# Kernel tuning notes

Measured on AMD Instinct MI355X. Metric: run time of the kernel, lower is better.

Reference implementation:

```python
import jax, jax.numpy as jnp
import numpy as np

N = 100000      # nodes
E = 1600000     # edges (avg degree 16)
F_IN = 128      # num_features
H = 128         # hidden_channels
OUT = 64        # out_channels


def _glorot(key, shape):
    lim = float(np.sqrt(6.0 / (shape[0] + shape[1])))
    return jax.random.uniform(key, shape, jnp.float32, -lim, lim)


def setup_inputs() -> dict:
    key = jax.random.key(0)
    ks = jax.random.split(key, 5)
    x = jax.random.normal(ks[0], (N, F_IN), jnp.float32)
    edge_index = jax.random.randint(ks[1], (2, E), 0, N, dtype=jnp.int64)
    W1 = _glorot(ks[2], (F_IN, H)); b1 = jnp.zeros((H,), jnp.float32)
    W2 = _glorot(ks[3], (H, H));    b2 = jnp.zeros((H,), jnp.float32)
    W3 = _glorot(ks[4], (H, OUT));  b3 = jnp.zeros((OUT,), jnp.float32)
    return {"x": x, "edge_index": edge_index,
            "W1": W1, "b1": b1, "W2": W2, "b2": b2, "W3": W3, "b3": b3}


def _gcn_conv(h, src, dst, norm, W, b, n):
    # PyG GCNConv: linear transform, then sym-normalized scatter aggregation, then bias
    h = h @ W                                   # [N, d_out]
    msg = h[src] * norm[:, None]                # gather + scale, [E+N, d_out]
    agg = jax.ops.segment_sum(msg, dst, num_segments=n)
    return agg + b


def reference(x, edge_index, W1, b1, W2, b2, W3, b3):
    n = x.shape[0]
    # add self-loops (GCNConv default add_self_loops=True)
    loop = jnp.arange(n, dtype=edge_index.dtype)
    src = jnp.concatenate([edge_index[0], loop])
    dst = jnp.concatenate([edge_index[1], loop])
    # symmetric normalization deg^-1/2[src] * deg^-1/2[dst]
    deg = jax.ops.segment_sum(jnp.ones_like(dst, x.dtype), dst, num_segments=n)
    dinv = jnp.where(deg > 0, jax.lax.rsqrt(deg), 0.0)
    norm = dinv[src] * dinv[dst]

    h = jax.nn.relu(_gcn_conv(x, src, dst, norm, W1, b1, n))  # dropout p=0 -> no-op
    h = jax.nn.relu(_gcn_conv(h, src, dst, norm, W2, b2, n))
    h = _gcn_conv(h, src, dst, norm, W3, b3, n)
    return jax.nn.log_softmax(h, axis=1)
```

## Files before the change

### kernel.cpp

```cpp
#include <hip/hip_runtime.h>
#include <stdint.h>
#include <math.h>

#define FIN 128

typedef __attribute__((ext_vector_type(8))) short short8v;
typedef __attribute__((ext_vector_type(4))) float float4v;
typedef __attribute__((ext_vector_type(2))) float float2v;

__device__ __forceinline__ uint32_t f2_to_bf2(float x, float y) {
    uint32_t r;
    asm("v_cvt_pk_bf16_f32 %0, %1, %2" : "=v"(r) : "v"(x), "v"(y));
    return r;
}
__device__ __forceinline__ unsigned short f_to_bf(float x) {
    union { float f; uint32_t i; } a;
    a.f = x;
    uint32_t u = a.i + 0x7FFF + ((a.i >> 16) & 1);
    return (unsigned short)(u >> 16);
}
__device__ __forceinline__ void acc16_fp8_pk(float2v* acc2, uint4 v) {
    uint32_t us[4] = {v.x, v.y, v.z, v.w};
#pragma unroll
    for (int q = 0; q < 4; ++q) {
        acc2[q * 2 + 0] += __builtin_amdgcn_cvt_pk_f32_fp8(us[q], false);
        acc2[q * 2 + 1] += __builtin_amdgcn_cvt_pk_f32_fp8(us[q], true);
    }
}

__device__ __forceinline__ int edge_at(const void* ei, long long idx, int is32) {
    return is32 ? ((const int*)ei)[idx] : (int)((const long long*)ei)[idx];
}

#define SP_CHUNK 4096
__global__ __launch_bounds__(256) void splitA_kernel(const void* __restrict__ ei,
                                                     int* __restrict__ gCnt,
                                                     uint32_t* __restrict__ buf1,
                                                     int E, int capS) {
    __shared__ int hist[16];
    __shared__ int gbase[16];
    __shared__ int lflag;
    int t = threadIdx.x;
    if (t < 16) hist[t] = 0;
    if (t == 0) lflag = 0;
    long long base = (long long)blockIdx.x * SP_CHUNK;
    __syncthreads();
    {
        long long e = base + t;
        if (e < E && ((const int*)ei)[2 * e + 1] != 0) atomicOr(&lflag, 1);
    }
    __syncthreads();
    int is32 = lflag;
    uint32_t lrec[16], rec[16];
#pragma unroll
    for (int j = 0; j < 16; ++j) {
        long long e = base + t + j * 256;
        if (e < E) {
            int s = edge_at(ei, e, is32);
            int d = edge_at(ei, (long long)E + e, is32);
            int b = d >> 13;
            int lofs = atomicAdd(&hist[b], 1);
            lrec[j] = ((uint32_t)lofs << 4) | (uint32_t)b;
            rec[j] = ((uint32_t)s << 13) | (uint32_t)(d & 8191);
        } else
            lrec[j] = 0xFFFFFFFFu;
    }
    __syncthreads();
    if (t < 16) gbase[t] = atomicAdd(&gCnt[t], hist[t]);
    __syncthreads();
#pragma unroll
    for (int j = 0; j < 16; ++j) {
        if (lrec[j] != 0xFFFFFFFFu) {
            int b = lrec[j] & 15;
            int pos = gbase[b] + (int)(lrec[j] >> 4);
            if (pos < capS) buf1[(size_t)b * capS + pos] = rec[j];
        }
    }
}

__global__ __launch_bounds__(256) void splitB_kernel(const int* __restrict__ gCnt,
                                                     const uint32_t* __restrict__ buf1,
                                                     int* __restrict__ cnt2,
                                                     uint32_t* __restrict__ buf2,
                                                     int capS, int cap2, int NB) {
    __shared__ int hist[128];
    __shared__ int gbase[128];
    int t = threadIdx.x;
    int s = blockIdx.y;
    if (t < 128) hist[t] = 0;
    __syncthreads();
    int m = gCnt[s];
    if (m > capS) m = capS;
    long long base = (long long)blockIdx.x * SP_CHUNK;
    uint32_t lrec[16], r32[16];
#pragma unroll
    for (int j = 0; j < 16; ++j) {
        long long i = base + t + j * 256;
        if (i < m) {
            uint32_t r = buf1[(size_t)s * capS + i];
            int d13 = (int)(r & 8191u);
            int sub = d13 >> 6;
            int lofs = atomicAdd(&hist[sub], 1);
            lrec[j] = ((uint32_t)lofs << 7) | (uint32_t)sub;
            r32[j] = ((r >> 13) << 6) | (uint32_t)(d13 & 63);
        } else
            lrec[j] = 0xFFFFFFFFu;
    }
    __syncthreads();
    if (t < 128) {
        int g = s * 128 + t;
        gbase[t] = (g < NB) ? atomicAdd(&cnt2[g], hist[t]) : 0;
    }
    __syncthreads();
#pragma unroll
    for (int j = 0; j < 16; ++j) {
        if (lrec[j] != 0xFFFFFFFFu) {
            int sub = lrec[j] & 127;
            int pos = gbase[sub] + (int)(lrec[j] >> 7);
            if (pos < cap2) buf2[(size_t)(s * 128 + sub) * cap2 + pos] = r32[j];
        }
    }
}

__global__ __launch_bounds__(256) void binBC_kernel(const int* __restrict__ cnt2,
                                                    const uint32_t* __restrict__ buf2,
                                                    int* __restrict__ cnt,
                                                    float* __restrict__ dinv,
                                                    int* __restrict__ rowend,
                                                    int* __restrict__ col,
                                                    int n, int cap2) {
    __shared__ int h[64];
    __shared__ int rowst[64];
    __shared__ int cur[64];
    __shared__ int sc[64];
    int bin = blockIdx.x;
    int t = threadIdx.x;
    if (t < 64) { h[t] = 0; cur[t] = 0; }
    __syncthreads();
    int m = cnt2[bin];
    if (m > cap2) m = cap2;
    const uint32_t* buf = buf2 + (size_t)bin * cap2;
    for (int i = t; i < m; i += 256) atomicAdd(&h[buf[i] & 63], 1);
    __syncthreads();
    int c = 0;
    if (t < 64) { c = h[t]; sc[t] = c; }
    __syncthreads();
    for (int off = 1; off < 64; off <<= 1) {
        int v = 0;
        if (t < 64 && t >= off) v = sc[t - off];
        __syncthreads();
        if (t < 64) sc[t] += v;
        __syncthreads();
    }
    if (t < 64) {
        int node = bin * 64 + t;
        int base = bin * cap2;
        rowst[t] = base + sc[t] - c;
        if (node < n) {
            cnt[node] = c;
            dinv[node] = rsqrtf((float)c + 1.0f);
            rowend[node] = base + sc[t];
        }
    }
    __syncthreads();
    for (int i = t; i < m; i += 256) {
        uint32_t rec = buf[i];
        int d6 = rec & 63;
        int off = atomicAdd(&cur[d6], 1);
        col[rowst[d6] + off] = (int)(rec >> 6);
    }
}

__global__ __launch_bounds__(256) void wconv_all(const float* __restrict__ W1,
                                                 const float* __restrict__ W2,
                                                 const float* __restrict__ W3,
                                                 unsigned short* __restrict__ Wf1,
                                                 unsigned short* __restrict__ Wf2,
                                                 unsigned short* __restrict__ Wf3) {
    int idx = blockIdx.x * 256 + threadIdx.x;
    const float* W;
    unsigned short* Wf;
    int NCOL, base;
    if (idx < 2048)      { W = W1; Wf = Wf1; NCOL = 128; base = idx; }
    else if (idx < 4096) { W = W2; Wf = Wf2; NCOL = 128; base = idx - 2048; }
    else if (idx < 5120) { W = W3; Wf = Wf3; NCOL = 64;  base = idx - 4096; }
    else return;
    int f = base >> 6, l = base & 63;
    int ct = f >> 2, ks = f & 3;
    int nn = ct * 16 + (l & 15);
    int k0 = ks * 32 + (l >> 4) * 8;
    uint32_t pk[4];
#pragma unroll
    for (int j = 0; j < 4; ++j) {
        float a = W[(size_t)(k0 + 2 * j) * NCOL + nn];
        float b = W[(size_t)(k0 + 2 * j + 1) * NCOL + nn];
        pk[j] = f2_to_bf2(a, b);
    }
    uint4 v = make_uint4(pk[0], pk[1], pk[2], pk[3]);
    ((uint4*)Wf)[base] = v;
}

template <int NCOL, int A_FP32, int OUT_FP8>
__global__ __launch_bounds__(256) void gemm_mfma(const void* __restrict__ Av,
                                                 const unsigned short* __restrict__ Wf,
                                                 const float* __restrict__ dinv,
                                                 void* __restrict__ Cv, int n) {
    __shared__ unsigned short lds[NCOL * 128];
    const int t = threadIdx.x;
    for (int i = t; i < NCOL * 16; i += 256)
        ((uint4*)lds)[i] = ((const uint4*)Wf)[i];
    __syncthreads();

    const int wave = t >> 6, lane = t & 63;
    const int row0 = blockIdx.x * 64 + wave * 16;
    const int m = lane & 15, quad = lane >> 4;
    int arow = row0 + m;
    if (arow >= n) arow = n - 1;

    short8v a[4];
    if (A_FP32) {
        const float* A = (const float*)Av;
#pragma unroll
        for (int ks = 0; ks < 4; ++ks) {
            float4 lo = *(const float4*)(A + (size_t)arow * 128 + ks * 32 + quad * 8);
            float4 hi = *(const float4*)(A + (size_t)arow * 128 + ks * 32 + quad * 8 + 4);
            union { short8v v; uint32_t u[4]; } pk;
            pk.u[0] = f2_to_bf2(lo.x, lo.y);
            pk.u[1] = f2_to_bf2(lo.z, lo.w);
            pk.u[2] = f2_to_bf2(hi.x, hi.y);
            pk.u[3] = f2_to_bf2(hi.z, hi.w);
            a[ks] = pk.v;
        }
    } else {
        const unsigned short* A = (const unsigned short*)Av;
#pragma unroll
        for (int ks = 0; ks < 4; ++ks)
            a[ks] = *(const short8v*)(A + (size_t)arow * 128 + ks * 32 + quad * 8);
    }

    const int cr0 = row0 + quad * 4;
    float ds[4];
#pragma unroll
    for (int r = 0; r < 4; ++r) {
        int gr = cr0 + r;
        ds[r] = (gr < n) ? dinv[gr] : 0.0f;
    }
#pragma unroll
    for (int ct = 0; ct < NCOL / 16; ++ct) {
        float4v acc = {0.0f, 0.0f, 0.0f, 0.0f};
#pragma unroll
        for (int ks = 0; ks < 4; ++ks) {
            int f = ct * 4 + ks;
            short8v b = *(const short8v*)(lds + ((size_t)(f * 64 + lane)) * 8);
            acc = __builtin_amdgcn_mfma_f32_16x16x32_bf16(a[ks], b, acc, 0, 0, 0);
        }
#pragma unroll
        for (int r = 0; r < 4; ++r) {
            int gr = cr0 + r;
            if (gr < n) {
                float val = acc[r] * ds[r];
                if (OUT_FP8) {
                    int u = __builtin_amdgcn_cvt_pk_fp8_f32(val, val, 0, false);
                    ((unsigned char*)Cv)[(size_t)gr * NCOL + ct * 16 + m] =
                        (unsigned char)(u & 0xFF);
                } else {
                    ((unsigned short*)Cv)[(size_t)gr * NCOL + ct * 16 + m] = f_to_bf(val);
                }
            }
        }
    }
}

__global__ __launch_bounds__(256) void agg_relu_128_fp8(
        const uint32_t* __restrict__ T8, const int* __restrict__ rowend,
        const int* __restrict__ cnt, const int* __restrict__ col,
        const float* __restrict__ dinv, const float* __restrict__ bias,
        uint32_t* __restrict__ outHb, int n) {
    int wid = blockIdx.x * 4 + (threadIdx.x >> 6);
    int lane = threadIdx.x & 63;
    int sel = lane >> 5, slot = (lane >> 3) & 3, j = lane & 7;
    int nodeA = wid * 2;
    int node = nodeA + sel;
    if (nodeA >= n) return;
    bool valid = node < n;
    int nd = valid ? node : nodeA;
    int end = rowend[nd];
    int start = end - cnt[nd];
    if (!valid) start = end;

    float2v acc2[8];
#pragma unroll
    for (int k = 0; k < 8; ++k) acc2[k] = (float2v){0.0f, 0.0f};
    if (slot == 0 && valid) {
        uint4 v = *(const uint4*)(T8 + (size_t)node * 32 + j * 4);
        acc16_fp8_pk(acc2, v);
    }
    int deg = end - start;
    int degM = max(deg, __shfl_xor(deg, 32, 64));
    int p = start + slot;
    const int ZR = n;
    for (int it = 0; it < degM; it += 8) {
        int e0 = p, e1 = p + 4;
        int s0 = col[e0], s1 = col[e1];
        if (e0 >= end) s0 = ZR;
        if (e1 >= end) s1 = ZR;
        uint4 v0 = *(const uint4*)(T8 + (size_t)s0 * 32 + j * 4);
        uint4 v1 = *(const uint4*)(T8 + (size_t)s1 * 32 + j * 4);
        acc16_fp8_pk(acc2, v0);
        acc16_fp8_pk(acc2, v1);
        p += 8;
    }
    float* acc = (float*)acc2;
#pragma unroll
    for (int k = 0; k < 16; ++k) {
        acc[k] += __shfl_xor(acc[k], 8, 64);
        acc[k] += __shfl_xor(acc[k], 16, 64);
    }
    if (slot == 0 && valid) {
        float di = dinv[node];
        const float4* b4 = (const float4*)bias;
        float r[16];
#pragma unroll
        for (int q = 0; q < 4; ++q) {
            float4 bb = b4[j * 4 + q];
            r[q * 4 + 0] = fmaxf(di * acc[q * 4 + 0] + bb.x, 0.0f);
            r[q * 4 + 1] = fmaxf(di * acc[q * 4 + 1] + bb.y, 0.0f);
            r[q * 4 + 2] = fmaxf(di * acc[q * 4 + 2] + bb.z, 0.0f);
            r[q * 4 + 3] = fmaxf(di * acc[q * 4 + 3] + bb.w, 0.0f);
        }
        uint4 o0, o1;
        o0.x = f2_to_bf2(r[0], r[1]);   o0.y = f2_to_bf2(r[2], r[3]);
        o0.z = f2_to_bf2(r[4], r[5]);   o0.w = f2_to_bf2(r[6], r[7]);
        o1.x = f2_to_bf2(r[8], r[9]);   o1.y = f2_to_bf2(r[10], r[11]);
        o1.z = f2_to_bf2(r[12], r[13]); o1.w = f2_to_bf2(r[14], r[15]);
        *(uint4*)(outHb + (size_t)node * 64 + j * 8) = o0;
        *(uint4*)(outHb + (size_t)node * 64 + j * 8 + 4) = o1;
    }
}

__global__ __launch_bounds__(256) void agg_lsm_64_fp8(
        const uint32_t* __restrict__ T8, const int* __restrict__ rowend,
        const int* __restrict__ cnt, const int* __restrict__ col,
        const float* __restrict__ dinv, const float* __restrict__ bias,
        float* __restrict__ out, int n) {
    int wid = blockIdx.x * 4 + (threadIdx.x >> 6);
    int lane = threadIdx.x & 63;
    int sel = lane >> 5, slot = (lane >> 2) & 7, j = lane & 3;
    int nodeA = wid * 2;
    int node = nodeA + sel;
    if (nodeA >= n) return;
    bool valid = node < n;
    int nd = valid ? node : nodeA;
    int end = rowend[nd];
    int start = end - cnt[nd];
    if (!valid) start = end;

    float2v acc2[8];
#pragma unroll
    for (int k = 0; k < 8; ++k) acc2[k] = (float2v){0.0f, 0.0f};
    if (slot == 0 && valid) {
        uint4 v = *(const uint4*)(T8 + (size_t)node * 16 + j * 4);
        acc16_fp8_pk(acc2, v);
    }
    int deg = end - start;
    int degM = max(deg, __shfl_xor(deg, 32, 64));
    int p = start + slot;
    const int ZR = 2 * n;
    for (int it = 0; it < degM; it += 16) {
        int e0 = p, e1 = p + 8;
        int s0 = col[e0], s1 = col[e1];
        if (e0 >= end) s0 = ZR;
        if (e1 >= end) s1 = ZR;
        uint4 v0 = *(const uint4*)(T8 + (size_t)s0 * 16 + j * 4);
        uint4 v1 = *(const uint4*)(T8 + (size_t)s1 * 16 + j * 4);
        acc16_fp8_pk(acc2, v0);
        acc16_fp8_pk(acc2, v1);
        p += 16;
    }
    float* acc = (float*)acc2;
#pragma unroll
    for (int k = 0; k < 16; ++k) {
        acc[k] += __shfl_xor(acc[k], 4, 64);
        acc[k] += __shfl_xor(acc[k], 8, 64);
        acc[k] += __shfl_xor(acc[k], 16, 64);
    }
    float di = dinv[nd];
    const float4* b4 = (const float4*)bias;
    float r[16];
#pragma unroll
    for (int q = 0; q < 4; ++q) {
        float4 bb = b4[j * 4 + q];
        r[q * 4 + 0] = di * acc[q * 4 + 0] + bb.x;
        r[q * 4 + 1] = di * acc[q * 4 + 1] + bb.y;
        r[q * 4 + 2] = di * acc[q * 4 + 2] + bb.z;
        r[q * 4 + 3] = di * acc[q * 4 + 3] + bb.w;
    }
    float m8[8];
#pragma unroll
    for (int q = 0; q < 8; ++q) m8[q] = fmaxf(r[2 * q], r[2 * q + 1]);
#pragma unroll
    for (int q = 0; q < 4; ++q) m8[q] = fmaxf(m8[q], m8[q + 4]);
    float m = fmaxf(fmaxf(m8[0], m8[2]), fmaxf(m8[1], m8[3]));
    m = fmaxf(m, __shfl_xor(m, 1, 64));
    m = fmaxf(m, __shfl_xor(m, 2, 64));
    float e[16];
#pragma unroll
    for (int k = 0; k < 16; ++k) e[k] = __expf(r[k] - m);
#pragma unroll
    for (int q = 0; q < 8; ++q) e[q] += e[q + 8];
#pragma unroll
    for (int q = 0; q < 4; ++q) e[q] += e[q + 4];
    float ss = (e[0] + e[2]) + (e[1] + e[3]);
    ss += __shfl_xor(ss, 1, 64);
    ss += __shfl_xor(ss, 2, 64);
    float lg = m + __logf(ss);
    if (slot == 0 && valid) {
#pragma unroll
        for (int q = 0; q < 4; ++q) {
            float4 o = make_float4(r[q * 4 + 0] - lg, r[q * 4 + 1] - lg,
                                   r[q * 4 + 2] - lg, r[q * 4 + 3] - lg);
            *(float4*)(out + (size_t)node * 64 + j * 16 + q * 4) = o;
        }
    }
}

extern "C" void kernel_launch(void* const* d_in, const int* in_sizes, int n_in,
                              void* d_out, int out_size, void* d_ws, size_t ws_size,
                              hipStream_t stream) {
    const float* x  = (const float*)d_in[0];
    const void*  ei = d_in[1];
    const float* W1 = (const float*)d_in[2];
    const float* b1 = (const float*)d_in[3];
    const float* W2 = (const float*)d_in[4];
    const float* b2 = (const float*)d_in[5];
    const float* W3 = (const float*)d_in[6];
    const float* b3 = (const float*)d_in[7];
    float* out = (float*)d_out;

    const int n = in_sizes[0] / FIN;
    const int E = in_sizes[1] / 2;

    char* p = (char*)d_ws;
    auto carve = [&](size_t bytes) {
        char* q = p;
        p += (bytes + 255) & ~(size_t)255;
        return q;
    };
    const int NB = (n + 63) / 64;
    const int NS = (n + 8191) / 8192;

    long long meanS = (long long)E * 8192 / n;
    int capS = (int)(meanS + 8 * (long long)sqrt((double)meanS) + 1024);
    capS = (capS + 15) & ~15;
    long long mean2 = (long long)E * 64 / n;
    int cap2 = (int)(mean2 + 8 * (long long)sqrt((double)mean2) + 64);
    cap2 = (cap2 + 15) & ~15;

    int*   cnt     = (int*)carve((size_t)n * 4);
    int*   rowend  = (int*)carve((size_t)n * 4);
    float* dinv    = (float*)carve((size_t)n * 4);
    int*   colb    = (int*)carve(((size_t)NB * cap2 + 4096) * 4);
    int*   gCnt    = (int*)carve((size_t)(16 + NB) * 4);
    int*   cnt2    = gCnt + 16;
    size_t Tbytes = (size_t)n * 128 + 256;
    size_t Hbytes = (size_t)n * 128 * 2;
    char*  TH = carve(Tbytes + Hbytes);
    void*  T  = (void*)TH;
    unsigned short* Hb = (unsigned short*)(TH + Tbytes);
    unsigned short* Wf1 = (unsigned short*)carve(128 * 128 * 2);
    unsigned short* Wf2 = (unsigned short*)carve(128 * 128 * 2);
    unsigned short* Wf3 = (unsigned short*)carve(128 * 64 * 2);

    size_t buf1B = ((size_t)NS * capS * 4 + 255) & ~(size_t)255;
    uint32_t* buf1 = (uint32_t*)TH;
    uint32_t* buf2 = (uint32_t*)(TH + buf1B);
    size_t avail2 = (Tbytes + Hbytes > buf1B) ? (Tbytes + Hbytes - buf1B) : 0;
    size_t maxc2 = avail2 / ((size_t)NB * 4);
    if ((size_t)cap2 > maxc2) cap2 = (int)maxc2;

    hipMemsetAsync(gCnt, 0, (size_t)(16 + NB) * 4, stream);

    const int gagg2 = ((n + 1) / 2 + 3) / 4;
    const int ggemm = (n + 63) / 64;
    const int gsplitA = (E + SP_CHUNK - 1) / SP_CHUNK;
    const int gsplitBx = (capS + SP_CHUNK - 1) / SP_CHUNK;

    splitA_kernel<<<gsplitA, 256, 0, stream>>>(ei, gCnt, buf1, E, capS);
    splitB_kernel<<<dim3(gsplitBx, NS), 256, 0, stream>>>(gCnt, buf1, cnt2, buf2, capS,
                                                          cap2, NB);
    binBC_kernel<<<NB, 256, 0, stream>>>(cnt2, buf2, cnt, dinv, rowend, colb, n, cap2);
    hipMemsetAsync(TH + (size_t)n * 128, 0, 128, stream);
    wconv_all<<<20, 256, 0, stream>>>(W1, W2, W3, Wf1, Wf2, Wf3);

    gemm_mfma<128, 1, 1><<<ggemm, 256, 0, stream>>>(x, Wf1, dinv, T, n);
    agg_relu_128_fp8<<<gagg2, 256, 0, stream>>>((const uint32_t*)T, rowend, cnt, colb,
                                                dinv, b1, (uint32_t*)Hb, n);
    gemm_mfma<128, 0, 1><<<ggemm, 256, 0, stream>>>(Hb, Wf2, dinv, T, n);
    agg_relu_128_fp8<<<gagg2, 256, 0, stream>>>((const uint32_t*)T, rowend, cnt, colb,
                                                dinv, b2, (uint32_t*)Hb, n);
    gemm_mfma<64, 0, 1><<<ggemm, 256, 0, stream>>>(Hb, Wf3, dinv, T, n);
    agg_lsm_64_fp8<<<gagg2, 256, 0, stream>>>((const uint32_t*)T, rowend, cnt, colb,
                                              dinv, b3, out, n);
}
```

Before: 297.8 us.

## Store self-loop and pad CSR rows to multiples of four, regather aggregation lanes

The CSR build now puts each node's self-loop into its own column list and pads every row to a multiple of four with a zero-row index, so cnt includes the self-loop and dinv uses rsqrt(cnt). The aggregation kernels loop over padded rows with no per-edge bounds checks and no separate self-term load. Lanes are remapped to two or four edge slots with 8-byte gathers, and the slot reduction uses DPP and ds_swizzle instead of shuffles. The zero row is now written by the GEMM kernel instead of a memset, and cap2 grows to hold the padding, which costs extra column storage and some padded gather work.

Measured after the change: 323.1 us. +8.5%, slower.

```diff
diff --git a/kernel.cpp b/kernel.cpp
--- a/kernel.cpp
+++ b/kernel.cpp
@@ -19,13 +19,22 @@
     uint32_t u = a.i + 0x7FFF + ((a.i >> 16) & 1);
     return (unsigned short)(u >> 16);
 }
-__device__ __forceinline__ void acc16_fp8_pk(float2v* acc2, uint4 v) {
-    uint32_t us[4] = {v.x, v.y, v.z, v.w};
-#pragma unroll
-    for (int q = 0; q < 4; ++q) {
-        acc2[q * 2 + 0] += __builtin_amdgcn_cvt_pk_f32_fp8(us[q], false);
-        acc2[q * 2 + 1] += __builtin_amdgcn_cvt_pk_f32_fp8(us[q], true);
-    }
+__device__ __forceinline__ void acc8_fp8_pk(float2v* acc2, uint2 v) {
+    acc2[0] += __builtin_amdgcn_cvt_pk_f32_fp8(v.x, false);
+    acc2[1] += __builtin_amdgcn_cvt_pk_f32_fp8(v.x, true);
+    acc2[2] += __builtin_amdgcn_cvt_pk_f32_fp8(v.y, false);
+    acc2[3] += __builtin_amdgcn_cvt_pk_f32_fp8(v.y, true);
+}
+
+template <int CTRL>
+__device__ __forceinline__ float dppmov(float x) {
+    int i = __builtin_bit_cast(int, x);
+    int r = __builtin_amdgcn_update_dpp(i, i, CTRL, 0xF, 0xF, false);
+    return __builtin_bit_cast(float, r);
+}
+__device__ __forceinline__ float swz16f(float x) {
+    int r = __builtin_amdgcn_ds_swizzle(__builtin_bit_cast(int, x), 0x401F);
+    return __builtin_bit_cast(float, r);
 }
 
 __device__ __forceinline__ int edge_at(const void* ei, long long idx, int is32) {
@@ -126,7 +135,7 @@
                                                     const uint32_t* __restrict__ buf2,
                                                     int* __restrict__ cnt,
                                                     float* __restrict__ dinv,
-                                                    int* __restrict__ rowend,
+                                                    int* __restrict__ rowstart,
                                                     int* __restrict__ col,
                                                     int n, int cap2) {
     __shared__ int h[64];
@@ -135,15 +144,18 @@
     __shared__ int sc[64];
     int bin = blockIdx.x;
     int t = threadIdx.x;
-    if (t < 64) { h[t] = 0; cur[t] = 0; }
+    if (t < 64) {
+        h[t] = (bin * 64 + t < n) ? 1 : 0;
+        cur[t] = 1;
+    }
     __syncthreads();
     int m = cnt2[bin];
     if (m > cap2) m = cap2;
     const uint32_t* buf = buf2 + (size_t)bin * cap2;
     for (int i = t; i < m; i += 256) atomicAdd(&h[buf[i] & 63], 1);
     __syncthreads();
-    int c = 0;
-    if (t < 64) { c = h[t]; sc[t] = c; }
+    int c = 0, pc = 0;
+    if (t < 64) { c = h[t]; pc = (c + 3) & ~3; sc[t] = pc; }
     __syncthreads();
     for (int off = 1; off < 64; off <<= 1) {
         int v = 0;
@@ -155,11 +167,14 @@
     if (t < 64) {
         int node = bin * 64 + t;
         int base = bin * cap2;
-        rowst[t] = base + sc[t] - c;
+        int st = base + sc[t] - pc;
+        rowst[t] = st;
         if (node < n) {
             cnt[node] = c;
-            dinv[node] = rsqrtf((float)c + 1.0f);
-            rowend[node] = base + sc[t];
+            dinv[node] = rsqrtf((float)c);
+            rowstart[node] = st;
+            col[st] = node;
+            for (int k = c; k < pc; ++k) col[st + k] = n;
         }
     }
     __syncthreads();
@@ -207,6 +222,8 @@
                                                  void* __restrict__ Cv, int n) {
     __shared__ unsigned short lds[NCOL * 128];
     const int t = threadIdx.x;
+    if (blockIdx.x == 0 && t < NCOL / 4)
+        ((uint32_t*)Cv)[(size_t)n * (NCOL / 4) + t] = 0;
     for (int i = t; i < NCOL * 16; i += 256)
         ((uint4*)lds)[i] = ((const uint4*)Wf)[i];
     __syncthreads();
@@ -272,155 +289,124 @@
 }
 
 __global__ __launch_bounds__(256) void agg_relu_128_fp8(
-        const uint32_t* __restrict__ T8, const int* __restrict__ rowend,
+        const uint32_t* __restrict__ T8, const int* __restrict__ rowstart,
         const int* __restrict__ cnt, const int* __restrict__ col,
         const float* __restrict__ dinv, const float* __restrict__ bias,
         uint32_t* __restrict__ outHb, int n) {
     int wid = blockIdx.x * 4 + (threadIdx.x >> 6);
     int lane = threadIdx.x & 63;
-    int sel = lane >> 5, slot = (lane >> 3) & 3, j = lane & 7;
+    int slot = lane & 1, j = (lane >> 1) & 15, sel = lane >> 5;
     int nodeA = wid * 2;
     int node = nodeA + sel;
     if (nodeA >= n) return;
     bool valid = node < n;
     int nd = valid ? node : nodeA;
-    int end = rowend[nd];
-    int start = end - cnt[nd];
-    if (!valid) start = end;
-
-    float2v acc2[8];
-#pragma unroll
-    for (int k = 0; k < 8; ++k) acc2[k] = (float2v){0.0f, 0.0f};
+    int start = rowstart[nd];
+    int c = cnt[nd];
+    int pend = start + ((c + 3) & ~3);
+    if (!valid) pend = start;
+
+    float2v acc2[4];
+#pragma unroll
+    for (int k = 0; k < 4; ++k) acc2[k] = (float2v){0.0f, 0.0f};
+    const uint2* T2 = (const uint2*)T8;
+    for (int p = start; p < pend; p += 4) {
+        int s0 = col[p + slot];
+        int s1 = col[p + slot + 2];
+        uint2 v0 = T2[(size_t)s0 * 16 + j];
+        uint2 v1 = T2[(size_t)s1 * 16 + j];
+        acc8_fp8_pk(acc2, v0);
+        acc8_fp8_pk(acc2, v1);
+    }
+    float* acc = (float*)acc2;
+#pragma unroll
+    for (int k = 0; k < 8; ++k) acc[k] += dppmov<0xB1>(acc[k]);
+    float di = dinv[nd];
+    const float4* b4 = (const float4*)bias;
+    float4 bb0 = b4[j * 2], bb1 = b4[j * 2 + 1];
+    float r[8];
+    r[0] = fmaxf(di * acc[0] + bb0.x, 0.0f);
+    r[1] = fmaxf(di * acc[1] + bb0.y, 0.0f);
+    r[2] = fmaxf(di * acc[2] + bb0.z, 0.0f);
+    r[3] = fmaxf(di * acc[3] + bb0.w, 0.0f);
+    r[4] = fmaxf(di * acc[4] + bb1.x, 0.0f);
+    r[5] = fmaxf(di * acc[5] + bb1.y, 0.0f);
+    r[6] = fmaxf(di * acc[6] + bb1.z, 0.0f);
+    r[7] = fmaxf(di * acc[7] + bb1.w, 0.0f);
     if (slot == 0 && valid) {
-        uint4 v = *(const uint4*)(T8 + (size_t)node * 32 + j * 4);
-        acc16_fp8_pk(acc2, v);
-    }
-    int deg = end - start;
-    int degM = max(deg, __shfl_xor(deg, 32, 64));
-    int p = start + slot;
-    const int ZR = n;
-    for (int it = 0; it < degM; it += 8) {
-        int e0 = p, e1 = p + 4;
-        int s0 = col[e0], s1 = col[e1];
-        if (e0 >= end) s0 = ZR;
-        if (e1 >= end) s1 = ZR;
-        uint4 v0 = *(const uint4*)(T8 + (size_t)s0 * 32 + j * 4);
-        uint4 v1 = *(const uint4*)(T8 + (size_t)s1 * 32 + j * 4);
-        acc16_fp8_pk(acc2, v0);
-        acc16_fp8_pk(acc2, v1);
-        p += 8;
-    }
-    float* acc = (float*)acc2;
-#pragma unroll
-    for (int k = 0; k < 16; ++k) {
-        acc[k] += __shfl_xor(acc[k], 8, 64);
-        acc[k] += __shfl_xor(acc[k], 16, 64);
-    }
-    if (slot == 0 && valid) {
-        float di = dinv[node];
-        const float4* b4 = (const float4*)bias;
-        float r[16];
-#pragma unroll
-        for (int q = 0; q < 4; ++q) {
-            float4 bb = b4[j * 4 + q];
-            r[q * 4 + 0] = fmaxf(di * acc[q * 4 + 0] + bb.x, 0.0f);
-            r[q * 4 + 1] = fmaxf(di * acc[q * 4 + 1] + bb.y, 0.0f);
-            r[q * 4 + 2] = fmaxf(di * acc[q * 4 + 2] + bb.z, 0.0f);
-            r[q * 4 + 3] = fmaxf(di * acc[q * 4 + 3] + bb.w, 0.0f);
-        }
-        uint4 o0, o1;
-        o0.x = f2_to_bf2(r[0], r[1]);   o0.y = f2_to_bf2(r[2], r[3]);
-        o0.z = f2_to_bf2(r[4], r[5]);   o0.w = f2_to_bf2(r[6], r[7]);
-        o1.x = f2_to_bf2(r[8], r[9]);   o1.y = f2_to_bf2(r[10], r[11]);
-        o1.z = f2_to_bf2(r[12], r[13]); o1.w = f2_to_bf2(r[14], r[15]);
-        *(uint4*)(outHb + (size_t)node * 64 + j * 8) = o0;
-        *(uint4*)(outHb + (size_t)node * 64 + j * 8 + 4) = o1;
+        uint4 o;
+        o.x = f2_to_bf2(r[0], r[1]);
+        o.y = f2_to_bf2(r[2], r[3]);
+        o.z = f2_to_bf2(r[4], r[5]);
+        o.w = f2_to_bf2(r[6], r[7]);
+        *(uint4*)(outHb + (size_t)node * 64 + j * 4) = o;
     }
 }
 
 __global__ __launch_bounds__(256) void agg_lsm_64_fp8(
-        const uint32_t* __restrict__ T8, const int* __restrict__ rowend,
+        const uint32_t* __restrict__ T8, const int* __restrict__ rowstart,
         const int* __restrict__ cnt, const int* __restrict__ col,
         const float* __restrict__ dinv, const float* __restrict__ bias,
         float* __restrict__ out, int n) {
     int wid = blockIdx.x * 4 + (threadIdx.x >> 6);
     int lane = threadIdx.x & 63;
-    int sel = lane >> 5, slot = (lane >> 2) & 7, j = lane & 3;
+    int slot = lane & 3, j = (lane >> 2) & 7, sel = lane >> 5;
     int nodeA = wid * 2;
     int node = nodeA + sel;
     if (nodeA >= n) return;
     bool valid = node < n;
     int nd = valid ? node : nodeA;
-    int end = rowend[nd];
-    int start = end - cnt[nd];
-    if (!valid) start = end;
-
-    float2v acc2[8];
-#pragma unroll
-    for (int k = 0; k < 8; ++k) acc2[k] = (float2v){0.0f, 0.0f};
-    if (slot == 0 && valid) {
-        uint4 v = *(const uint4*)(T8 + (size_t)node * 16 + j * 4);
-        acc16_fp8_pk(acc2, v);
-    }
-    int deg = end - start;
-    int degM = max(deg, __shfl_xor(deg, 32, 64));
-    int p = start + slot;
-    const int ZR = 2 * n;
-    for (int it = 0; it < degM; it += 16) {
-        int e0 = p, e1 = p + 8;
-        int s0 = col[e0], s1 = col[e1];
-        if (e0 >= end) s0 = ZR;
-        if (e1 >= end) s1 = ZR;
-        uint4 v0 = *(const uint4*)(T8 + (size_t)s0 * 16 + j * 4);
-        uint4 v1 = *(const uint4*)(T8 + (size_t)s1 * 16 + j * 4);
-        acc16_fp8_pk(acc2, v0);
-        acc16_fp8_pk(acc2, v1);
-        p += 16;
+    int start = rowstart[nd];
+    int c = cnt[nd];
+    int pend = start + ((c + 3) & ~3);
+    if (!valid) pend = start;
+
+    float2v acc2[4];
+#pragma unroll
+    for (int k = 0; k < 4; ++k) acc2[k] = (float2v){0.0f, 0.0f};
+    const uint2* T2 = (const uint2*)T8;
+    for (int p = start; p < pend; p += 4) {
+        int s0 = col[p + slot];
+        uint2 v0 = T2[(size_t)s0 * 8 + j];
+        acc8_fp8_pk(acc2, v0);
     }
     float* acc = (float*)acc2;
 #pragma unroll
-    for (int k = 0; k < 16; ++k) {
-        acc[k] += __shfl_xor(acc[k], 4, 64);
-        acc[k] += __shfl_xor(acc[k], 8, 64);
-        acc[k] += __shfl_xor(acc[k], 16, 64);
-    }
+    for (int k = 0; k < 8; ++k) acc[k] += dppmov<0xB1>(acc[k]);
+#pragma unroll
+    for (int k = 0; k < 8; ++k) acc[k] += dppmov<0x4E>(acc[k]);
     float di = dinv[nd];
     const float4* b4 = (const float4*)bias;
-    float r[16];
-#pragma unroll
-    for (int q = 0; q < 4; ++q) {
-        float4 bb = b4[j * 4 + q];
-        r[q * 4 + 0] = di * acc[q * 4 + 0] + bb.x;
-        r[q * 4 + 1] = di * acc[q * 4 + 1] + bb.y;
-        r[q * 4 + 2] = di * acc[q * 4 + 2] + bb.z;
-        r[q * 4 + 3] = di * acc[q * 4 + 3] + bb.w;
-    }
-    float m8[8];
-#pragma unroll
-    for (int q = 0; q < 8; ++q) m8[q] = fmaxf(r[2 * q], r[2 * q + 1]);
-#pragma unroll
-    for (int q = 0; q < 4; ++q) m8[q] = fmaxf(m8[q], m8[q + 4]);
-    float m = fmaxf(fmaxf(m8[0], m8[2]), fmaxf(m8[1], m8[3]));
-    m = fmaxf(m, __shfl_xor(m, 1, 64));
-    m = fmaxf(m, __shfl_xor(m, 2, 64));
-    float e[16];
-#pragma unroll
-    for (int k = 0; k < 16; ++k) e[k] = __expf(r[k] - m);
-#pragma unroll
-    for (int q = 0; q < 8; ++q) e[q] += e[q + 8];
-#pragma unroll
-    for (int q = 0; q < 4; ++q) e[q] += e[q + 4];
-    float ss = (e[0] + e[2]) + (e[1] + e[3]);
-    ss += __shfl_xor(ss, 1, 64);
-    ss += __shfl_xor(ss, 2, 64);
+    float4 bb0 = b4[j * 2], bb1 = b4[j * 2 + 1];
+    float r[8];
+    r[0] = di * acc[0] + bb0.x;
+    r[1] = di * acc[1] + bb0.y;
+    r[2] = di * acc[2] + bb0.z;
+    r[3] = di * acc[3] + bb0.w;
+    r[4] = di * acc[4] + bb1.x;
+    r[5] = di * acc[5] + bb1.y;
+    r[6] = di * acc[6] + bb1.z;
+    r[7] = di * acc[7] + bb1.w;
+    float m0 = fmaxf(fmaxf(r[0], r[1]), fmaxf(r[2], r[3]));
+    float m1 = fmaxf(fmaxf(r[4], r[5]), fmaxf(r[6], r[7]));
+    float m = fmaxf(m0, m1);
+    m = fmaxf(m, dppmov<0x124>(m));
+    m = fmaxf(m, dppmov<0x128>(m));
+    m = fmaxf(m, swz16f(m));
+    float e0 = __expf(r[0] - m) + __expf(r[1] - m);
+    float e1 = __expf(r[2] - m) + __expf(r[3] - m);
+    float e2 = __expf(r[4] - m) + __expf(r[5] - m);
+    float e3 = __expf(r[6] - m) + __expf(r[7] - m);
+    float ss = (e0 + e1) + (e2 + e3);
+    ss += dppmov<0x124>(ss);
+    ss += dppmov<0x128>(ss);
+    ss += swz16f(ss);
     float lg = m + __logf(ss);
     if (slot == 0 && valid) {
-#pragma unroll
-        for (int q = 0; q < 4; ++q) {
-            float4 o = make_float4(r[q * 4 + 0] - lg, r[q * 4 + 1] - lg,
-                                   r[q * 4 + 2] - lg, r[q * 4 + 3] - lg);
-            *(float4*)(out + (size_t)node * 64 + j * 16 + q * 4) = o;
-        }
+        float4 o0 = make_float4(r[0] - lg, r[1] - lg, r[2] - lg, r[3] - lg);
+        float4 o1 = make_float4(r[4] - lg, r[5] - lg, r[6] - lg, r[7] - lg);
+        *(float4*)(out + (size_t)node * 64 + j * 8) = o0;
+        *(float4*)(out + (size_t)node * 64 + j * 8 + 4) = o1;
     }
 }
 
@@ -453,15 +439,15 @@
     int capS = (int)(meanS + 8 * (long long)sqrt((double)meanS) + 1024);
     capS = (capS + 15) & ~15;
     long long mean2 = (long long)E * 64 / n;
-    int cap2 = (int)(mean2 + 8 * (long long)sqrt((double)mean2) + 64);
+    int cap2 = (int)(mean2 + 8 * (long long)sqrt((double)mean2) + 832);
     cap2 = (cap2 + 15) & ~15;
 
-    int*   cnt     = (int*)carve((size_t)n * 4);
-    int*   rowend  = (int*)carve((size_t)n * 4);
-    float* dinv    = (float*)carve((size_t)n * 4);
-    int*   colb    = (int*)carve(((size_t)NB * cap2 + 4096) * 4);
-    int*   gCnt    = (int*)carve((size_t)(16 + NB) * 4);
-    int*   cnt2    = gCnt + 16;
+    int*   cnt      = (int*)carve((size_t)n * 4);
+    int*   rowstart = (int*)carve((size_t)n * 4);
+    float* dinv     = (float*)carve((size_t)n * 4);
+    int*   colb     = (int*)carve(((size_t)NB * cap2 + 4096) * 4);
+    int*   gCnt     = (int*)carve((size_t)(16 + NB) * 4);
+    int*   cnt2     = gCnt + 16;
     size_t Tbytes = (size_t)n * 128 + 256;
     size_t Hbytes = (size_t)n * 128 * 2;
     char*  TH = carve(Tbytes + Hbytes);
@@ -488,17 +474,17 @@
     splitA_kernel<<<gsplitA, 256, 0, stream>>>(ei, gCnt, buf1, E, capS);
     splitB_kernel<<<dim3(gsplitBx, NS), 256, 0, stream>>>(gCnt, buf1, cnt2, buf2, capS,
                                                           cap2, NB);
-    binBC_kernel<<<NB, 256, 0, stream>>>(cnt2, buf2, cnt, dinv, rowend, colb, n, cap2);
-    hipMemsetAsync(TH + (size_t)n * 128, 0, 128, stream);
+    binBC_kernel<<<NB, 256, 0, stream>>>(cnt2, buf2, cnt, dinv, rowstart, colb, n,
+                                         cap2);
     wconv_all<<<20, 256, 0, stream>>>(W1, W2, W3, Wf1, Wf2, Wf3);
 
     gemm_mfma<128, 1, 1><<<ggemm, 256, 0, stream>>>(x, Wf1, dinv, T, n);
-    agg_relu_128_fp8<<<gagg2, 256, 0, stream>>>((const uint32_t*)T, rowend, cnt, colb,
-                                                dinv, b1, (uint32_t*)Hb, n);
+    agg_relu_128_fp8<<<gagg2, 256, 0, stream>>>((const uint32_t*)T, rowstart, cnt,
+                                                colb, dinv, b1, (uint32_t*)Hb, n);
     gemm_mfma<128, 0, 1><<<ggemm, 256, 0, stream>>>(Hb, Wf2, dinv, T, n);
-    agg_relu_128_fp8<<<gagg2, 256, 0, stream>>>((const uint32_t*)T, rowend, cnt, colb,
-                                                dinv, b2, (uint32_t*)Hb, n);
+    agg_relu_128_fp8<<<gagg2, 256, 0, stream>>>((const uint32_t*)T, rowstart, cnt,
+                                                colb, dinv, b2, (uint32_t*)Hb, n);
     gemm_mfma<64, 0, 1><<<ggemm, 256, 0, stream>>>(Hb, Wf3, dinv, T, n);
-    agg_lsm_64_fp8<<<gagg2, 256, 0, stream>>>((const uint32_t*)T, rowend, cnt, colb,
+    agg_lsm_64_fp8<<<gagg2, 256, 0, stream>>>((const uint32_t*)T, rowstart, cnt, colb,
                                               dinv, b3, out, n);
 }
```
